# Kernel optimization log

Hardware: AMD Instinct MI355X
Metric: run time of the kernel (lower is better)

## Reference

```python
import jax, jax.numpy as jnp
import numpy as np

DEPTH = 3
HIDDEN = 300
ATOM_FDIM = 133
BOND_FDIM = 147


def setup_inputs() -> dict:
    key = jax.random.key(0)
    ks = jax.random.split(key, 10)
    n_atoms, n_bonds, max_nb, n_mols = 200000, 400000, 6, 10000
    f_atoms = jax.random.normal(ks[0], (n_atoms, ATOM_FDIM), dtype=jnp.float32)
    f_bonds = jax.random.normal(ks[1], (n_bonds, BOND_FDIM), dtype=jnp.float32)
    a2b = jax.random.randint(ks[2], (n_atoms, max_nb), 0, n_bonds)
    b2a = jax.random.randint(ks[3], (n_bonds,), 0, n_atoms)
    b2revb = jax.random.randint(ks[4], (n_bonds,), 0, n_bonds)
    # learned parameters (fan-in scaled)
    W_i = jax.random.normal(ks[5], (BOND_FDIM, HIDDEN), dtype=jnp.float32) / np.sqrt(BOND_FDIM)
    W_h = jax.random.normal(ks[6], (HIDDEN, HIDDEN), dtype=jnp.float32) / np.sqrt(HIDDEN)
    W_o = jax.random.normal(ks[7], (ATOM_FDIM + HIDDEN, HIDDEN), dtype=jnp.float32) / np.sqrt(ATOM_FDIM + HIDDEN)
    b_o = jnp.zeros((HIDDEN,), dtype=jnp.float32)
    return {"f_atoms": f_atoms, "f_bonds": f_bonds, "a2b": a2b, "b2a": b2a,
            "b2revb": b2revb, "W_i": W_i, "W_h": W_h, "W_o": W_o, "b_o": b_o,
            "n_mols": n_mols}


def reference(f_atoms, f_bonds, a2b, b2a, b2revb, W_i, W_h, W_o, b_o, n_mols):
    act = jax.nn.relu
    # input = W_i(f_bonds); message = act(input)
    inp = f_bonds @ W_i                       # [n_bonds, H]
    message = act(inp)
    for _ in range(DEPTH - 1):
        nei_a_message = message[a2b]          # [n_atoms, max_nb, H] gather
        a_message = nei_a_message.sum(axis=1)  # [n_atoms, H]
        rev_message = message[b2revb]         # [n_bonds, H]
        message = a_message[b2a] - rev_message
        message = act(inp + message @ W_h)
    # final atom readout
    a_message = message[a2b].sum(axis=1)      # [n_atoms, H]
    a_input = jnp.concatenate([f_atoms, a_message], axis=1)
    atom_hiddens = act(a_input @ W_o + b_o)   # [n_atoms, H]
    # scope-based mean pooling (uniform molecules: n_atoms = n_mols * apm)
    apm = f_atoms.shape[0] // n_mols
    mol_vecs = atom_hiddens.reshape(n_mols, apm, HIDDEN).mean(axis=1)
    return mol_vecs
```

## Files before the change

### kernel.cpp

```cpp
#include <hip/hip_runtime.h>
#include <hip/hip_bf16.h>
#include <cstdint>
#include <cstddef>

#define HP 320

typedef unsigned short ushortT;
typedef __attribute__((ext_vector_type(8))) __bf16 bf16x8;
typedef __attribute__((ext_vector_type(4))) float f32x4;

__device__ __forceinline__ float b2f(unsigned u) {
    union { unsigned i; float f; } v; v.i = u << 16; return v.f;
}
__device__ __forceinline__ ushortT f2b(float f) {
    union { float f; unsigned i; } v; v.f = f;
    unsigned x = v.i;
    return (ushortT)((x + 0x7fffu + ((x >> 16) & 1u)) >> 16);
}
__device__ __forceinline__ unsigned subpk(unsigned a, unsigned r) {
    union { unsigned i; float f; } al, ah, rl, rh;
    al.i = a << 16; ah.i = a & 0xffff0000u;
    rl.i = r << 16; rh.i = r & 0xffff0000u;
    float lo = al.f - rl.f, hi = ah.f - rh.f;
    return (unsigned)f2b(lo) | ((unsigned)f2b(hi) << 16);
}
__device__ __forceinline__ uint4 subpk4(uint4 a, uint4 r) {
    uint4 o;
    o.x = subpk(a.x, r.x); o.y = subpk(a.y, r.y);
    o.z = subpk(a.z, r.z); o.w = subpk(a.w, r.w);
    return o;
}
__device__ __forceinline__ void upadd(uint4 u, float* s) {
    s[0] += b2f(u.x & 0xffff); s[1] += b2f(u.x >> 16);
    s[2] += b2f(u.y & 0xffff); s[3] += b2f(u.y >> 16);
    s[4] += b2f(u.z & 0xffff); s[5] += b2f(u.z >> 16);
    s[6] += b2f(u.w & 0xffff); s[7] += b2f(u.w >> 16);
}
__device__ __forceinline__ uint4 pk8(const float* s) {
    uint4 o;
    o.x = (unsigned)f2b(s[0]) | ((unsigned)f2b(s[1]) << 16);
    o.y = (unsigned)f2b(s[2]) | ((unsigned)f2b(s[3]) << 16);
    o.z = (unsigned)f2b(s[4]) | ((unsigned)f2b(s[5]) << 16);
    o.w = (unsigned)f2b(s[6]) | ((unsigned)f2b(s[7]) << 16);
    return o;
}

__device__ __forceinline__ void pack_one(int idx, const float* __restrict__ W,
                                         int Ksrc, ushortT* __restrict__ dst) {
    int j = idx & 7, col = (idx >> 3) & 15, kg = (idx >> 7) & 3;
    int t = idx >> 9; int nt = t % 20, kt = t / 20;
    int k = kt * 32 + kg * 8 + j, n = nt * 16 + col;
    float v = (k < Ksrc && n < 300) ? W[k * 300 + n] : 0.f;
    dst[idx] = f2b(v);
}
__device__ __forceinline__ void pack_wo(int idx, const float* __restrict__ W,
                                        ushortT* __restrict__ dst) {
    int j = idx & 7, col = (idx >> 3) & 15, kg = (idx >> 7) & 3;
    int t = idx >> 9; int nt = t % 20, kt = t / 20;
    int k = kt * 32 + kg * 8 + j, n = nt * 16 + col;
    int src = (k < 133) ? k : ((k >= 160 && k < 460) ? (k - 27) : -1);
    float v = (src >= 0 && n < 300) ? W[src * 300 + n] : 0.f;
    dst[idx] = f2b(v);
}

__global__ __launch_bounds__(256) void k_pack_weights(
    const float* __restrict__ Wi, const float* __restrict__ Wh,
    const float* __restrict__ Wo, const float* __restrict__ bo,
    ushortT* __restrict__ Wipk, ushortT* __restrict__ Whpk,
    ushortT* __restrict__ Wopk, float* __restrict__ bop) {
    int idx = blockIdx.x * 256 + threadIdx.x;
    if (idx < 51200)  pack_one(idx, Wi, 147, Wipk);
    if (idx < 102400) pack_one(idx, Wh, 300, Whpk);
    if (idx < 153600) pack_wo(idx, Wo, Wopk);
    if (idx < HP) bop[idx] = (idx < 300) ? bo[idx] : 0.f;
}

template <int MODE, bool AUXP>
__global__ __launch_bounds__(256, 3) void k_mfma(
    const float* __restrict__ fa, const float* __restrict__ fb,
    const ushortT* __restrict__ aux,
    const ushortT* __restrict__ amsg,
    const ushortT* __restrict__ msgin,
    const int* __restrict__ b2a, const int* __restrict__ b2revb,
    const ushortT* __restrict__ Bpk1, const ushortT* __restrict__ Bpk2,
    const float* __restrict__ bop,
    ushortT* __restrict__ outp,
    ushortT* __restrict__ auxw) {
    constexpr int KT = (MODE == 0) ? 5 : 15;
    constexpr int SPLIT = (MODE == 1) ? 10 : KT;
    constexpr int SP = (MODE == 0) ? 168 : ((MODE == 1) ? 328 : 488);
    __shared__ __align__(16) ushortT panel[64 * SP];
    __shared__ int idxA[(MODE == 1) ? 64 : 1];
    __shared__ int idxR[(MODE == 1) ? 64 : 1];

    const int tid = threadIdx.x, wave = tid >> 6, lane = tid & 63;
    const int row0 = blockIdx.x * 64;
    const int kg8 = (lane >> 4) * 8;
    const int l15 = lane & 15;

    if (MODE == 1) {
        if (tid < 64) {
            idxA[tid] = b2a[row0 + tid];
            idxR[tid] = b2revb[row0 + tid];
        }
        __syncthreads();
    }

    f32x4 acc[4][5];
#pragma unroll
    for (int i = 0; i < 4; i++)
#pragma unroll
        for (int n = 0; n < 5; n++) acc[i][n] = (f32x4){0.f, 0.f, 0.f, 0.f};

    uint4 breg[2][5];
    const int boff = wave * 5 * 512 + (lane >> 4) * 128 + l15 * 8;

#define LOADB(kt, buf)                                                               \
    {                                                                                \
        const ushortT* bp = ((kt) < SPLIT) ? (Bpk1 + (size_t)(kt) * 10240)           \
                                           : (Bpk2 + (size_t)((kt) - SPLIT) * 10240);\
        _Pragma("unroll")                                                            \
        for (int n = 0; n < 5; n++)                                                  \
            breg[buf][n] = *(const uint4*)(bp + boff + n * 512);                     \
    }

#define MSTEP(bufi, pk0)                                                             \
    {                                                                                \
        bf16x8 a0 = *(bf16x8*)&panel[(l15) * SP + (pk0) + kg8];                      \
        bf16x8 a1 = *(bf16x8*)&panel[(16 + l15) * SP + (pk0) + kg8];                 \
        bf16x8 a2 = *(bf16x8*)&panel[(32 + l15) * SP + (pk0) + kg8];                 \
        bf16x8 a3 = *(bf16x8*)&panel[(48 + l15) * SP + (pk0) + kg8];                 \
        __builtin_amdgcn_s_setprio(1);                                               \
        _Pragma("unroll")                                                            \
        for (int n = 0; n < 5; n++) {                                                \
            bf16x8 b;                                                                \
            *(uint4*)&b = breg[bufi][n];                                             \
            acc[0][n] = __builtin_amdgcn_mfma_f32_16x16x32_bf16(b, a0, acc[0][n], 0, 0, 0); \
            acc[1][n] = __builtin_amdgcn_mfma_f32_16x16x32_bf16(b, a1, acc[1][n], 0, 0, 0); \
            acc[2][n] = __builtin_amdgcn_mfma_f32_16x16x32_bf16(b, a2, acc[2][n], 0, 0, 0); \
            acc[3][n] = __builtin_amdgcn_mfma_f32_16x16x32_bf16(b, a3, acc[3][n], 0, 0, 0); \
        }                                                                            \
        __builtin_amdgcn_s_setprio(0);                                               \
    }

#define BUILD_FEAT(src, FD, row, ch, vout)                                           \
    {                                                                                \
        union { ushortT u[8]; uint4 w; } t;                                          \
        _Pragma("unroll")                                                            \
        for (int j = 0; j < 8; j++) {                                                \
            int k = (ch) * 8 + j;                                                    \
            t.u[j] = (k < FD) ? f2b(src[(size_t)(row) * FD + k]) : (ushortT)0;       \
        }                                                                            \
        vout = t.w;                                                                  \
    }

    if (MODE == 0) {
#pragma unroll
        for (int it = 0; it < 5; it++) {
            int flat = tid + 256 * it;
            int row = flat / 20, ch = flat - row * 20;
            uint4 v;
            BUILD_FEAT(fb, 147, row0 + row, ch, v);
            *(uint4*)&panel[row * SP + ch * 8] = v;
            if (AUXP) *(uint4*)(auxw + (size_t)(row0 + row) * 160 + ch * 8) = v;
        }
        LOADB(0, 0);
        __syncthreads();
#pragma unroll
        for (int kt = 0; kt < 5; kt++) {
            if (kt + 1 < 5) LOADB(kt + 1, (kt + 1) & 1);
            MSTEP(kt & 1, kt * 32);
        }
    } else if (MODE == 1) {
#pragma unroll
        for (int it = 0; it < 5; it++) {
            int flat = tid + 256 * it;
            int row = flat / 20, ch = flat - row * 20;
            uint4 ua = *(const uint4*)(amsg + (size_t)idxA[row] * HP + ch * 8);
            uint4 ur = *(const uint4*)(msgin + (size_t)idxR[row] * HP + ch * 8);
            *(uint4*)&panel[row * SP + ch * 8] = subpk4(ua, ur);
        }
        LOADB(0, 0);
        __syncthreads();
#pragma unroll
        for (int kt = 0; kt < 5; kt++) {
            LOADB(kt + 1, (kt + 1) & 1);
            int flat = tid + 256 * kt;
            int srow = flat / 20, sch = flat - srow * 20;
            uint4 ua = *(const uint4*)(amsg + (size_t)idxA[srow] * HP + 160 + sch * 8);
            uint4 ur = *(const uint4*)(msgin + (size_t)idxR[srow] * HP + 160 + sch * 8);
            MSTEP(kt & 1, kt * 32);
            *(uint4*)&panel[srow * SP + 160 + sch * 8] = subpk4(ua, ur);
        }
        __syncthreads();
#pragma unroll
        for (int kt = 5; kt < 10; kt++) {
            LOADB(kt + 1, (kt + 1) & 1);
            int flat = tid + 256 * (kt - 5);
            int srow = flat / 20, sch = flat - srow * 20;
            uint4 v;
            if (AUXP) {
                v = *(const uint4*)(aux + (size_t)(row0 + srow) * 160 + sch * 8);
                MSTEP(kt & 1, kt * 32);
            } else {
                BUILD_FEAT(fb, 147, row0 + srow, sch, v);
                MSTEP(kt & 1, kt * 32);
            }
            *(uint4*)&panel[srow * SP + sch * 8] = v;
        }
        __syncthreads();
#pragma unroll
        for (int kt = 10; kt < 15; kt++) {
            if (kt + 1 < 15) LOADB(kt + 1, (kt + 1) & 1);
            MSTEP(kt & 1, (kt - 10) * 32);
        }
    } else {
#pragma unroll
        for (int it = 0; it < 5; it++) {
            int flat = tid + 256 * it;
            int row = flat / 20, ch = flat - row * 20;
            uint4 v;
            BUILD_FEAT(fa, 133, row0 + row, ch, v);
            *(uint4*)&panel[row * SP + ch * 8] = v;
        }
        LOADB(0, 0);
        __syncthreads();
#pragma unroll
        for (int kt = 0; kt < 5; kt++) {
            LOADB(kt + 1, (kt + 1) & 1);
            int f0 = tid + 256 * (2 * kt), f1 = tid + 256 * (2 * kt + 1);
            int r0 = f0 / 40, c0 = f0 - r0 * 40;
            int r1 = f1 / 40, c1 = f1 - r1 * 40;
            uint4 v0 = *(const uint4*)(amsg + (size_t)(row0 + r0) * HP + c0 * 8);
            uint4 v1 = *(const uint4*)(amsg + (size_t)(row0 + r1) * HP + c1 * 8);
            MSTEP(kt & 1, kt * 32);
            *(uint4*)&panel[r0 * SP + 160 + c0 * 8] = v0;
            *(uint4*)&panel[r1 * SP + 160 + c1 * 8] = v1;
        }
        __syncthreads();
#pragma unroll
        for (int kt = 5; kt < 15; kt++) {
            if (kt + 1 < 15) LOADB(kt + 1, (kt + 1) & 1);
            MSTEP(kt & 1, kt * 32);
        }
    }
#undef LOADB
#undef MSTEP
#undef BUILD_FEAT

#pragma unroll
    for (int i = 0; i < 4; i++) {
        size_t gr = (size_t)(row0 + i * 16 + l15);
#pragma unroll
        for (int n = 0; n < 5; n++) {
            int col = wave * 80 + n * 16 + (lane >> 4) * 4;
            float4 v = make_float4(acc[i][n][0], acc[i][n][1], acc[i][n][2], acc[i][n][3]);
            if (MODE == 2) {
                float4 bias = *(const float4*)&bop[col];
                v.x += bias.x; v.y += bias.y; v.z += bias.z; v.w += bias.w;
            }
            ushort4 u;
            u.x = f2b(fmaxf(v.x, 0.f)); u.y = f2b(fmaxf(v.y, 0.f));
            u.z = f2b(fmaxf(v.z, 0.f)); u.w = f2b(fmaxf(v.w, 0.f));
            *(ushort4*)&outp[gr * HP + col] = u;
        }
    }
}

__global__ __launch_bounds__(256) void k_atom_sum(
    const ushortT* __restrict__ msg, const int* __restrict__ a2b,
    ushortT* __restrict__ amsg, int nA) {
    int t = blockIdx.x * 256 + threadIdx.x;
    int a = t / 40, q = t - a * 40;
    if (a >= nA) return;
    float s[8];
#pragma unroll
    for (int e = 0; e < 8; e++) s[e] = 0.f;
#pragma unroll
    for (int j = 0; j < 6; j++) {
        int b = a2b[a * 6 + j];
        uint4 u = *(const uint4*)(msg + (size_t)b * HP + q * 8);
        upadd(u, s);
    }
    *(uint4*)(amsg + (size_t)a * HP + q * 8) = pk8(s);
}

__global__ __launch_bounds__(256) void k_pool(
    const ushortT* __restrict__ ah, float* __restrict__ out, int n_mols, int apm) {
    int t = blockIdx.x * 256 + threadIdx.x;
    int m = t / 75, c4 = t - m * 75;
    if (m >= n_mols) return;
    float4 s = make_float4(0, 0, 0, 0);
    for (int u = 0; u < apm; u++) {
        ushort4 q = *(const ushort4*)&ah[(size_t)(m * apm + u) * HP + c4 * 4];
        s.x += b2f(q.x); s.y += b2f(q.y); s.z += b2f(q.z); s.w += b2f(q.w);
    }
    float inv = 1.0f / (float)apm;
    s.x *= inv; s.y *= inv; s.z *= inv; s.w *= inv;
    *(float4*)&out[(size_t)m * 300 + c4 * 4] = s;
}

extern "C" void kernel_launch(void* const* d_in, const int* in_sizes, int n_in,
                              void* d_out, int out_size, void* d_ws, size_t ws_size,
                              hipStream_t stream) {
    const float* fa     = (const float*)d_in[0];
    const float* fb     = (const float*)d_in[1];
    const int*   a2b    = (const int*)d_in[2];
    const int*   b2a    = (const int*)d_in[3];
    const int*   b2revb = (const int*)d_in[4];
    const float* Wi     = (const float*)d_in[5];
    const float* Wh     = (const float*)d_in[6];
    const float* Wo     = (const float*)d_in[7];
    const float* bo     = (const float*)d_in[8];

    const int nA     = in_sizes[0] / 133;
    const int nB     = in_sizes[1] / 147;
    const int n_mols = out_size / 300;
    const int apm    = nA / n_mols;

    char* p = (char*)d_ws;
    ushortT* Wipk = (ushortT*)p;  p += (size_t)51200 * 2;
    ushortT* Whpk = (ushortT*)p;  p += (size_t)102400 * 2;
    ushortT* Wopk = (ushortT*)p;  p += (size_t)153600 * 2;
    float*   bop  = (float*)p;    p += (size_t)HP * 4;
    p = (char*)(((uintptr_t)p + 255) & ~(uintptr_t)255);

    const size_t msgBytes  = (size_t)nB * HP * 2;
    const size_t amsgBytes = (size_t)nA * HP * 2;
    const size_t fbbBytes  = (size_t)nB * 160 * 2;
    const size_t headBytes = (size_t)(p - (char*)d_ws);
    const bool use_fbb = ws_size >= headBytes + 2 * msgBytes + amsgBytes + fbbBytes;

    ushortT* msgA = (ushortT*)p;  p += msgBytes;
    ushortT* msgB = (ushortT*)p;  p += msgBytes;
    ushortT* amsg = (ushortT*)p;  p += amsgBytes;
    ushortT* fbb  = use_fbb ? (ushortT*)p : nullptr;
    ushortT* ah   = msgB;
    float*   out  = (float*)d_out;

    k_pack_weights<<<600, 256, 0, stream>>>(Wi, Wh, Wo, bo, Wipk, Whpk, Wopk, bop);

    const int asum_grid = (int)(((size_t)nA * 40 + 255) / 256);
    const int gB = nB / 64, gA = nA / 64;

    if (use_fbb)
        k_mfma<0, true ><<<gB, 256, 0, stream>>>(fa, fb, nullptr, nullptr, nullptr, nullptr, nullptr,
                                                 Wipk, Wipk, bop, msgA, fbb);
    else
        k_mfma<0, false><<<gB, 256, 0, stream>>>(fa, fb, nullptr, nullptr, nullptr, nullptr, nullptr,
                                                 Wipk, Wipk, bop, msgA, nullptr);

    k_atom_sum<<<asum_grid, 256, 0, stream>>>(msgA, a2b, amsg, nA);
    if (use_fbb)
        k_mfma<1, true ><<<gB, 256, 0, stream>>>(fa, fb, fbb, amsg, msgA, b2a, b2revb,
                                                 Whpk, Wipk, bop, msgB, nullptr);
    else
        k_mfma<1, false><<<gB, 256, 0, stream>>>(fa, fb, nullptr, amsg, msgA, b2a, b2revb,
                                                 Whpk, Wipk, bop, msgB, nullptr);

    k_atom_sum<<<asum_grid, 256, 0, stream>>>(msgB, a2b, amsg, nA);
    if (use_fbb)
        k_mfma<1, true ><<<gB, 256, 0, stream>>>(fa, fb, fbb, amsg, msgB, b2a, b2revb,
                                                 Whpk, Wipk, bop, msgA, nullptr);
    else
        k_mfma<1, false><<<gB, 256, 0, stream>>>(fa, fb, nullptr, amsg, msgB, b2a, b2revb,
                                                 Whpk, Wipk, bop, msgA, nullptr);

    k_atom_sum<<<asum_grid, 256, 0, stream>>>(msgA, a2b, amsg, nA);
    k_mfma<2, false><<<gA, 256, 0, stream>>>(fa, fb, nullptr, amsg, nullptr, nullptr, nullptr,
                                             Wopk, Wopk, bop, ah, nullptr);
    k_pool<<<((n_mols * 75) + 255) / 256, 256, 0, stream>>>(ah, out, n_mols, apm);
}
```

Before: 1.360 ms.

## Stage A panel loads fully before MFMA loops instead of interleaving

In mode 1, the full 320-wide gathered message difference is now loaded into the LDS panel up front, and the global loads that were interleaved with the MFMA steps are removed. The bond features are then loaded in a separate phase. In mode 2, the LDS panel shrinks from 488 to 264 columns by loading atom features plus the first part of the atom messages, then reusing the panel for the remaining message columns. The smaller panel lets more blocks fit per CU in mode 2. The cost is losing the overlap of global loads with MFMA compute and adding extra barriers.

```diff
diff --git a/kernel.cpp b/kernel.cpp
--- a/kernel.cpp
+++ b/kernel.cpp
@@ -88,7 +88,7 @@
     ushortT* __restrict__ auxw) {
     constexpr int KT = (MODE == 0) ? 5 : 15;
     constexpr int SPLIT = (MODE == 1) ? 10 : KT;
-    constexpr int SP = (MODE == 0) ? 168 : ((MODE == 1) ? 328 : 488);
+    constexpr int SP = (MODE == 0) ? 168 : ((MODE == 1) ? 328 : 264);
     __shared__ __align__(16) ushortT panel[64 * SP];
     __shared__ int idxA[(MODE == 1) ? 64 : 1];
     __shared__ int idxR[(MODE == 1) ? 64 : 1];
@@ -173,9 +173,9 @@
         }
     } else if (MODE == 1) {
 #pragma unroll
-        for (int it = 0; it < 5; it++) {
-            int flat = tid + 256 * it;
-            int row = flat / 20, ch = flat - row * 20;
+        for (int it = 0; it < 10; it++) {
+            int flat = tid + 256 * it;
+            int row = flat / 40, ch = flat - row * 40;
             uint4 ua = *(const uint4*)(amsg + (size_t)idxA[row] * HP + ch * 8);
             uint4 ur = *(const uint4*)(msgin + (size_t)idxR[row] * HP + ch * 8);
             *(uint4*)&panel[row * SP + ch * 8] = subpk4(ua, ur);
@@ -183,30 +183,22 @@
         LOADB(0, 0);
         __syncthreads();
 #pragma unroll
-        for (int kt = 0; kt < 5; kt++) {
+        for (int kt = 0; kt < 10; kt++) {
             LOADB(kt + 1, (kt + 1) & 1);
-            int flat = tid + 256 * kt;
-            int srow = flat / 20, sch = flat - srow * 20;
-            uint4 ua = *(const uint4*)(amsg + (size_t)idxA[srow] * HP + 160 + sch * 8);
-            uint4 ur = *(const uint4*)(msgin + (size_t)idxR[srow] * HP + 160 + sch * 8);
             MSTEP(kt & 1, kt * 32);
-            *(uint4*)&panel[srow * SP + 160 + sch * 8] = subpk4(ua, ur);
-        }
-        __syncthreads();
-#pragma unroll
-        for (int kt = 5; kt < 10; kt++) {
-            LOADB(kt + 1, (kt + 1) & 1);
-            int flat = tid + 256 * (kt - 5);
-            int srow = flat / 20, sch = flat - srow * 20;
+        }
+        __syncthreads();
+#pragma unroll
+        for (int it = 0; it < 5; it++) {
+            int flat = tid + 256 * it;
+            int row = flat / 20, ch = flat - row * 20;
             uint4 v;
             if (AUXP) {
-                v = *(const uint4*)(aux + (size_t)(row0 + srow) * 160 + sch * 8);
-                MSTEP(kt & 1, kt * 32);
+                v = *(const uint4*)(aux + (size_t)(row0 + row) * 160 + ch * 8);
             } else {
-                BUILD_FEAT(fb, 147, row0 + srow, sch, v);
-                MSTEP(kt & 1, kt * 32);
+                BUILD_FEAT(fb, 147, row0 + row, ch, v);
             }
-            *(uint4*)&panel[srow * SP + sch * 8] = v;
+            *(uint4*)&panel[row * SP + ch * 8] = v;
         }
         __syncthreads();
 #pragma unroll
@@ -216,32 +208,37 @@
         }
     } else {
 #pragma unroll
-        for (int it = 0; it < 5; it++) {
-            int flat = tid + 256 * it;
-            int row = flat / 20, ch = flat - row * 20;
+        for (int it = 0; it < 8; it++) {
+            int flat = tid + 256 * it;
+            int row = flat / 32, ch = flat - row * 32;
             uint4 v;
-            BUILD_FEAT(fa, 133, row0 + row, ch, v);
+            if (ch >= 20) {
+                v = *(const uint4*)(amsg + (size_t)(row0 + row) * HP + (ch - 20) * 8);
+            } else {
+                BUILD_FEAT(fa, 133, row0 + row, ch, v);
+            }
             *(uint4*)&panel[row * SP + ch * 8] = v;
         }
         LOADB(0, 0);
         __syncthreads();
 #pragma unroll
-        for (int kt = 0; kt < 5; kt++) {
+        for (int kt = 0; kt < 8; kt++) {
             LOADB(kt + 1, (kt + 1) & 1);
-            int f0 = tid + 256 * (2 * kt), f1 = tid + 256 * (2 * kt + 1);
-            int r0 = f0 / 40, c0 = f0 - r0 * 40;
-            int r1 = f1 / 40, c1 = f1 - r1 * 40;
-            uint4 v0 = *(const uint4*)(amsg + (size_t)(row0 + r0) * HP + c0 * 8);
-            uint4 v1 = *(const uint4*)(amsg + (size_t)(row0 + r1) * HP + c1 * 8);
             MSTEP(kt & 1, kt * 32);
-            *(uint4*)&panel[r0 * SP + 160 + c0 * 8] = v0;
-            *(uint4*)&panel[r1 * SP + 160 + c1 * 8] = v1;
-        }
-        __syncthreads();
-#pragma unroll
-        for (int kt = 5; kt < 15; kt++) {
+        }
+        __syncthreads();
+#pragma unroll
+        for (int it = 0; it < 7; it++) {
+            int flat = tid + 256 * it;
+            int row = flat / 28, ch = flat - row * 28;
+            uint4 v = *(const uint4*)(amsg + (size_t)(row0 + row) * HP + 96 + ch * 8);
+            *(uint4*)&panel[row * SP + ch * 8] = v;
+        }
+        __syncthreads();
+#pragma unroll
+        for (int kt = 8; kt < 15; kt++) {
             if (kt + 1 < 15) LOADB(kt + 1, (kt + 1) & 1);
-            MSTEP(kt & 1, kt * 32);
+            MSTEP(kt & 1, (kt - 8) * 32);
         }
     }
 #undef LOADB
```

After: 1.340 ms. Within noise of the previous version (-1.5%).
